# Performance work log

Hardware: AMD Instinct MI355X
Metric: run time of the kernel (lower is better)

## Reference

```python
import jax, jax.numpy as jnp
import numpy as np

N_NODES = 100000
N_EDGES = 1600000
N_GRAPHS = 256
DIMS = [128, 128, 128, 128]  # gcn_layers_dim -> 3 GCNConv layers


def setup_inputs() -> dict:
    key = jax.random.key(0)
    ks = jax.random.split(key, 12)
    inp = {
        "x": jax.random.normal(ks[0], (N_NODES, DIMS[0]), jnp.float32),
        "edge_index": jax.random.randint(ks[1], (2, N_EDGES), 0, N_NODES),
        "edge_weight": jax.random.uniform(ks[2], (N_EDGES,), jnp.float32),
        "batch": jnp.sort(jax.random.randint(ks[3], (N_NODES,), 0, N_GRAPHS)),
    }
    for i in range(3):
        fan_in = DIMS[i]
        scale = 1.0 / np.sqrt(fan_in)
        inp[f"W{i+1}"] = jax.random.uniform(ks[4 + 2 * i], (DIMS[i], DIMS[i + 1]),
                                             jnp.float32, -scale, scale)
        inp[f"b{i+1}"] = jax.random.uniform(ks[5 + 2 * i], (DIMS[i + 1],),
                                             jnp.float32, -scale, scale)
    return inp


def reference(x, edge_index, edge_weight, batch, W1, b1, W2, b2, W3, b3):
    n = x.shape[0]
    # PyG GCNConv: add self-loops with weight 1, symmetric normalization.
    loop = jnp.arange(n)
    row = jnp.concatenate([edge_index[0], loop])  # source nodes
    col = jnp.concatenate([edge_index[1], loop])  # target nodes (aggregation index)
    w = jnp.concatenate([edge_weight, jnp.ones((n,), x.dtype)])
    deg = jax.ops.segment_sum(w, col, num_segments=n)
    dinv = jnp.where(deg > 0, jax.lax.rsqrt(deg), jnp.zeros_like(deg))
    norm = dinv[row] * w * dinv[col]  # [E+N]

    # global_mean_pool setup
    counts = jax.ops.segment_sum(jnp.ones((n,), x.dtype), batch,
                                 num_segments=N_GRAPHS)
    counts = jnp.maximum(counts, 1.0)[:, None]

    def gcn_conv(h, W, b):
        hl = h @ W                      # linear projection first (PyG order)
        msg = hl[row] * norm[:, None]   # gather + edge scaling
        out = jax.ops.segment_sum(msg, col, num_segments=n)  # scatter-add
        return out + b

    embeddings = []
    h = x
    for W, b in ((W1, b1), (W2, b2), (W3, b3)):
        h = gcn_conv(h, W, b)
        h = jax.nn.relu(h)              # relu_layers_index = [0,1,2]
        emb = jax.ops.segment_sum(h, batch, num_segments=N_GRAPHS) / counts
        embeddings.append(emb)          # gep = global_mean_pool
    return tuple(embeddings)
```

## Files before the change

kernel.cpp:

```cpp
#include <hip/hip_runtime.h>


typedef short short8 __attribute__((ext_vector_type(8)));
typedef float f32x4  __attribute__((ext_vector_type(4)));

__device__ inline unsigned pack_bf16x2(float a, float b) {
    unsigned ua = __float_as_uint(a);
    ua = (ua + 0x7FFFu + ((ua >> 16) & 1u)) >> 16;
    unsigned ub = __float_as_uint(b);
    ub = (ub + 0x7FFFu + ((ub >> 16) & 1u)) >> 16;
    return ua | (ub << 16);
}
__device__ inline ushort bf16_1(float a) {
    unsigned ua = __float_as_uint(a);
    return (ushort)((ua + 0x7FFFu + ((ua >> 16) & 1u)) >> 16);
}
__device__ inline float bf_lo(unsigned u) { return __uint_as_float(u << 16); }
__device__ inline float bf_hi(unsigned u) { return __uint_as_float(u & 0xFFFF0000u); }

__global__ void k_prep(int* __restrict__ cnt, int N,
                       const int* __restrict__ batch, int* __restrict__ gb, int G,
                       const float* __restrict__ W0, const float* __restrict__ W1,
                       const float* __restrict__ W2, ushort* __restrict__ WbT) {
    int id = blockIdx.x * blockDim.x + threadIdx.x;
    if (id < N) cnt[id] = 0;
    if (id <= G) {
        int lo = 0, hi = N;
        while (lo < hi) { int mid = (lo + hi) >> 1; if (batch[mid] < id) lo = mid + 1; else hi = mid; }
        gb[id] = lo;
    }
    if (id < 3 * 16384) {
        int l = id >> 14;
        const float* W = (l == 0) ? W0 : ((l == 1) ? W1 : W2);
        int id2 = id & 16383;
        int n = id2 & 127, k = id2 >> 7;
        WbT[l * 16384 + n * 128 + k] = bf16_1(W[k * 128 + n]);
    }
}

__global__ void k_phase1(const int* __restrict__ ei, int* __restrict__ cnt,
                         int* __restrict__ epos, int E,
                         const float4* __restrict__ x4, uint2* __restrict__ xb2,
                         int nCast) {
    int tid = blockIdx.x * blockDim.x + threadIdx.x;
    if (tid < E) {
        int c = ei[E + tid];
        epos[tid] = atomicAdd(&cnt[c], 1);
    }
    int stride = gridDim.x * blockDim.x;
    for (int i = tid; i < nCast; i += stride) {
        float4 f = x4[i];
        uint2 v;
        v.x = pack_bf16x2(f.x, f.y);
        v.y = pack_bf16x2(f.z, f.w);
        xb2[i] = v;
    }
}

__global__ __launch_bounds__(1024) void k_scan1(const int* __restrict__ cnt,
                                                int* __restrict__ pre,
                                                int* __restrict__ bsum, int n) {
    __shared__ int wsum[16];
    int t = threadIdx.x, lane = t & 63, w = t >> 6;
    int i = blockIdx.x * 1024 + t;
    int v = (i < n) ? cnt[i] : 0;
    int x = v;
#pragma unroll
    for (int off = 1; off < 64; off <<= 1) {
        int y = __shfl_up(x, off, 64);
        if (lane >= off) x += y;
    }
    if (lane == 63) wsum[w] = x;
    __syncthreads();
    int woff = 0, tot = 0;
#pragma unroll
    for (int q = 0; q < 16; q++) { int s = wsum[q]; if (q < w) woff += s; tot += s; }
    if (i < n) pre[i] = woff + x - v;
    if (t == 0) bsum[blockIdx.x] = tot;
}

__global__ __launch_bounds__(128) void k_scan2(int* __restrict__ bsum, int nb,
                                               int* __restrict__ ptrv, int n) {
    __shared__ int ws[2];
    int t = threadIdx.x, lane = t & 63, w = t >> 6;
    int v = (t < nb) ? bsum[t] : 0;
    int x = v;
#pragma unroll
    for (int off = 1; off < 64; off <<= 1) {
        int y = __shfl_up(x, off, 64);
        if (lane >= off) x += y;
    }
    if (lane == 63) ws[w] = x;
    __syncthreads();
    int woff = (w == 1) ? ws[0] : 0;
    int tot = ws[0] + ws[1];
    if (t < nb) bsum[t] = woff + x - v;
    if (t == 0) ptrv[n] = tot;
}

__global__ void k_scatter(const int* __restrict__ ei, const float* __restrict__ ew,
                          const int* __restrict__ pre, const int* __restrict__ bsum,
                          int* __restrict__ ptrv, const int* __restrict__ epos,
                          int2* __restrict__ csr, int E, int N) {
    int e = blockIdx.x * blockDim.x + threadIdx.x;
    if (e < N) ptrv[e] = pre[e] + bsum[e >> 10];
    if (e >= E) return;
    int r = ei[e];
    int c = ei[E + e];
    int2 v; v.x = r; v.y = __float_as_int(ew[e]);
    csr[pre[c] + bsum[c >> 10] + epos[e]] = v;
}

__global__ __launch_bounds__(256) void k_degdinv(const int2* __restrict__ csr,
                                                 const int* __restrict__ ptrv,
                                                 float* __restrict__ dinv, int N) {
    int node = blockIdx.x * 8 + (threadIdx.x >> 5);
    int j = threadIdx.x & 31;
    if (node >= N) return;
    int e0 = ptrv[node], e1 = ptrv[node + 1];
    float s = (j == 0) ? 1.0f : 0.0f;
    for (int e = e0 + j; e < e1; e += 32) s += __int_as_float(csr[e].y);
#pragma unroll
    for (int off = 1; off < 32; off <<= 1) s += __shfl_xor(s, off, 64);
    if (j == 0) dinv[node] = rsqrtf(s);
}

__global__ __launch_bounds__(256) void k_norm(int2* __restrict__ csr,
                                              const int* __restrict__ ptrv,
                                              const float* __restrict__ dinv, int N) {
    int node = blockIdx.x * 8 + (threadIdx.x >> 5);
    int j = threadIdx.x & 31;
    if (node >= N) return;
    float dc = dinv[node];
    int e0 = ptrv[node], e1 = ptrv[node + 1];
    for (int e = e0 + j; e < e1; e += 32) {
        int2 m = csr[e];
        m.y = __float_as_int(dinv[m.x] * __int_as_float(m.y) * dc);
        csr[e] = m;
    }
}

__global__ __launch_bounds__(256) void k_gemm_mfma(const unsigned* __restrict__ Hb,
                                                   const ushort* __restrict__ WbT,
                                                   unsigned* __restrict__ O, int M) {
    __shared__ unsigned sOut[4 * 32 * 64];
    int lane = threadIdx.x & 63;
    int wv = threadIdx.x >> 6;
    int quad = lane >> 4;
    int mrow = lane & 15;
    int m0 = blockIdx.x * 128 + wv * 32;
    int r0 = m0 + mrow;
    int r1 = r0 + 16;
    int r0c = r0 < M ? r0 : M - 1;
    int r1c = r1 < M ? r1 : M - 1;

    short8 a0[4], a1[4];
#pragma unroll
    for (int s = 0; s < 4; s++) {
        a0[s] = *(const short8*)(Hb + (size_t)r0c * 64 + s * 16 + quad * 4);
        a1[s] = *(const short8*)(Hb + (size_t)r1c * 64 + s * 16 + quad * 4);
    }
    f32x4 acc0[8], acc1[8];
#pragma unroll
    for (int t = 0; t < 8; t++) {
        acc0[t] = (f32x4){0.f, 0.f, 0.f, 0.f};
        acc1[t] = (f32x4){0.f, 0.f, 0.f, 0.f};
    }
#pragma unroll
    for (int s = 0; s < 4; s++) {
#pragma unroll
        for (int t = 0; t < 8; t++) {
            short8 b = *(const short8*)(WbT + (t * 16 + mrow) * 128 + s * 32 + quad * 8);
            acc0[t] = __builtin_amdgcn_mfma_f32_16x16x32_bf16(a0[s], b, acc0[t], 0, 0, 0);
            acc1[t] = __builtin_amdgcn_mfma_f32_16x16x32_bf16(a1[s], b, acc1[t], 0, 0, 0);
        }
    }
    ushort* so = (ushort*)(sOut + wv * 32 * 64);
#pragma unroll
    for (int t = 0; t < 8; t++) {
#pragma unroll
        for (int r = 0; r < 4; r++) {
            int lr = quad * 4 + r;
            int c = t * 16 + mrow;
            so[lr * 128 + c] = bf16_1(acc0[t][r]);
            so[(lr + 16) * 128 + c] = bf16_1(acc1[t][r]);
        }
    }
    __syncthreads();
    const unsigned* si = sOut + wv * 32 * 64;
#pragma unroll 8
    for (int r = 0; r < 32; r++) {
        int row = m0 + r;
        if (row < M) O[(size_t)row * 64 + lane] = si[r * 64 + lane];
    }
}

__global__ __launch_bounds__(256) void k_agg(const unsigned* __restrict__ HL,
                                             const int* __restrict__ ptr,
                                             const int2* __restrict__ csr,
                                             const float* __restrict__ dinv,
                                             const float* __restrict__ bias,
                                             unsigned* __restrict__ Hout, int M) {
    __shared__ int2 sM[4 * 64];
    int node = (int)((blockIdx.x * blockDim.x + threadIdx.x) >> 6);
    if (node >= M) return;
    int lane = threadIdx.x & 63;
    int half = lane >> 5;
    int q = lane & 31;
    int2* mbase = &sM[(threadIdx.x >> 6) * 64];
    int e0 = ptr[node], e1 = ptr[node + 1];
    int deg = e1 - e0;
    int nbv = deg < 64 ? deg : 64;
    if (lane < nbv) mbase[lane] = csr[e0 + lane];
    const uint2* HL2 = (const uint2*)HL;
    float di = dinv[node];
    float sn = (half == 0) ? di * di : 0.f;
    uint2 us = HL2[(size_t)node * 32 + q];
    float a0 = sn * bf_lo(us.x), a1 = sn * bf_hi(us.x);
    float a2 = sn * bf_lo(us.y), a3 = sn * bf_hi(us.y);
    int j = half;
    for (; j + 16 <= nbv; j += 16) {
        int2 m[8]; uint2 u[8];
#pragma unroll
        for (int t = 0; t < 8; t++) m[t] = mbase[j + 2 * t];
#pragma unroll
        for (int t = 0; t < 8; t++) u[t] = HL2[(size_t)m[t].x * 32 + q];
#pragma unroll
        for (int t = 0; t < 8; t++) {
            float nv = __int_as_float(m[t].y);
            a0 += nv * bf_lo(u[t].x); a1 += nv * bf_hi(u[t].x);
            a2 += nv * bf_lo(u[t].y); a3 += nv * bf_hi(u[t].y);
        }
    }
    for (; j + 8 <= nbv; j += 8) {
        int2 m[4]; uint2 u[4];
#pragma unroll
        for (int t = 0; t < 4; t++) m[t] = mbase[j + 2 * t];
#pragma unroll
        for (int t = 0; t < 4; t++) u[t] = HL2[(size_t)m[t].x * 32 + q];
#pragma unroll
        for (int t = 0; t < 4; t++) {
            float nv = __int_as_float(m[t].y);
            a0 += nv * bf_lo(u[t].x); a1 += nv * bf_hi(u[t].x);
            a2 += nv * bf_lo(u[t].y); a3 += nv * bf_hi(u[t].y);
        }
    }
    for (; j < nbv; j += 2) {
        int2 m = mbase[j];
        uint2 u = HL2[(size_t)m.x * 32 + q];
        float nv = __int_as_float(m.y);
        a0 += nv * bf_lo(u.x); a1 += nv * bf_hi(u.x);
        a2 += nv * bf_lo(u.y); a3 += nv * bf_hi(u.y);
    }
    for (int e = e0 + 64 + half; e < e1; e += 2) {
        int2 m = csr[e];
        uint2 u = HL2[(size_t)m.x * 32 + q];
        float nv = __int_as_float(m.y);
        a0 += nv * bf_lo(u.x); a1 += nv * bf_hi(u.x);
        a2 += nv * bf_lo(u.y); a3 += nv * bf_hi(u.y);
    }
    a0 += __shfl_xor(a0, 32, 64);
    a1 += __shfl_xor(a1, 32, 64);
    a2 += __shfl_xor(a2, 32, 64);
    a3 += __shfl_xor(a3, 32, 64);
    float4 bv = ((const float4*)bias)[q];
    float r0 = fmaxf(a0 + bv.x, 0.f);
    float r1 = fmaxf(a1 + bv.y, 0.f);
    float r2 = fmaxf(a2 + bv.z, 0.f);
    float r3 = fmaxf(a3 + bv.w, 0.f);
    if (half == 0) {
        uint2 pv;
        pv.x = pack_bf16x2(r0, r1);
        pv.y = pack_bf16x2(r2, r3);
        ((uint2*)(Hout + (size_t)node * 64))[q] = pv;
    }
}

__global__ __launch_bounds__(256) void k_pool(const unsigned* __restrict__ HB,
                                              const int* __restrict__ gb,
                                              float* __restrict__ outp) {
    __shared__ float part[4][128];
    int g = blockIdx.x;
    int lane = threadIdx.x & 63, w = threadIdx.x >> 6;
    int s = gb[g], e = gb[g + 1];
    float ax = 0.f, ay = 0.f;
    for (int i = s + w; i < e; i += 4) {
        unsigned u = HB[(size_t)i * 64 + lane];
        ax += bf_lo(u); ay += bf_hi(u);
    }
    part[w][lane * 2] = ax;
    part[w][lane * 2 + 1] = ay;
    __syncthreads();
    if (threadIdx.x < 128) {
        float sum = part[0][threadIdx.x] + part[1][threadIdx.x]
                  + part[2][threadIdx.x] + part[3][threadIdx.x];
        float c = (float)(e - s);
        outp[g * 128 + threadIdx.x] = sum / fmaxf(c, 1.0f);
    }
}

extern "C" void kernel_launch(void* const* d_in, const int* in_sizes, int n_in,
                              void* d_out, int out_size, void* d_ws, size_t ws_size,
                              hipStream_t stream) {
    const float* x     = (const float*)d_in[0];
    const int*   ei    = (const int*)d_in[1];
    const float* ew    = (const float*)d_in[2];
    const int*   batch = (const int*)d_in[3];
    const float* Wt[3] = {(const float*)d_in[4], (const float*)d_in[6], (const float*)d_in[8]};
    const float* bt[3] = {(const float*)d_in[5], (const float*)d_in[7], (const float*)d_in[9]};
    float* out = (float*)d_out;

    const int D = 128;
    const int N = in_sizes[0] / D;
    const int E = in_sizes[2];
    const int G = out_size / (3 * D);

    char* p = (char*)d_ws;
    auto alloc = [&](size_t bytes) {
        void* r = (void*)p;
        p += (bytes + 255) & ~(size_t)255;
        return r;
    };
    int*      cnt    = (int*)alloc((size_t)N * 4);
    int*      ptr    = (int*)alloc((size_t)(N + 1) * 4);
    int*      pre    = (int*)alloc((size_t)N * 4);
    int*      bsum   = (int*)alloc((size_t)128 * 4);
    int*      gb     = (int*)alloc((size_t)(G + 1) * 4);
    float*    dinv   = (float*)alloc((size_t)N * 4);
    ushort*   WbT    = (ushort*)alloc((size_t)3 * 16384 * 2);
    int2*     csr    = (int2*)alloc((size_t)E * 8);
    unsigned* xb     = (unsigned*)alloc((size_t)N * 64 * 4);
    unsigned* bufHL  = (unsigned*)alloc((size_t)N * 64 * 4);
    unsigned* bufH   = (unsigned*)alloc((size_t)N * 64 * 4);
    int*      epos   = (int*)bufH;

    int nb = (N + 1023) / 1024;
    int prepWork = N > 3 * 16384 ? N : 3 * 16384;

    k_prep<<<(prepWork + 255) / 256, 256, 0, stream>>>(cnt, N, batch, gb, G,
                                                       Wt[0], Wt[1], Wt[2], WbT);
    k_phase1<<<(E + 255) / 256, 256, 0, stream>>>(ei, cnt, epos, E,
                                                  (const float4*)x, (uint2*)xb, N * 32);
    k_scan1<<<nb, 1024, 0, stream>>>(cnt, pre, bsum, N);
    k_scan2<<<1, 128, 0, stream>>>(bsum, nb, ptr, N);
    k_scatter<<<(E + 255) / 256, 256, 0, stream>>>(ei, ew, pre, bsum, ptr, epos,
                                                   csr, E, N);
    k_degdinv<<<(N + 7) / 8, 256, 0, stream>>>(csr, ptr, dinv, N);
    k_norm<<<(N + 7) / 8, 256, 0, stream>>>(csr, ptr, dinv, N);

    for (int l = 0; l < 3; l++) {
        const unsigned* hin = (l == 0) ? xb : bufH;
        k_gemm_mfma<<<(N + 127) / 128, 256, 0, stream>>>(hin, WbT + (size_t)l * 16384,
                                                         bufHL, N);
        k_agg<<<(N + 3) / 4, 256, 0, stream>>>(bufHL, ptr, csr, dinv, bt[l], bufH, N);
        k_pool<<<G, 256, 0, stream>>>(bufH, gb, out + (size_t)l * G * D);
    }
}
```

Before: 613.2 us.

## Fuse first GEMM with edge counting, merge scan2 into scatter, co-launch GEMM and pool

The separate fp32-to-bf16 cast pass over x is removed. The layer-0 GEMM now reads fp32 x directly, converts it in registers, and runs in the same grid as the edge-count atomics. The second scan stage is folded into the scatter kernel, with each block redundantly re-scanning the 128 block sums. Each later layer's GEMM shares one launch with the previous layer's pooling. The 16-wide unrolled edge loop in aggregation is also dropped. Together these cut launches and a full-size intermediate buffer round-trip, at the cost of heterogeneous blocks in the fused grids and a smaller unroll in the gather loop.

```diff
diff --git a/kernel.cpp b/kernel.cpp
--- a/kernel.cpp
+++ b/kernel.cpp
@@ -18,12 +18,111 @@
 __device__ inline float bf_lo(unsigned u) { return __uint_as_float(u << 16); }
 __device__ inline float bf_hi(unsigned u) { return __uint_as_float(u & 0xFFFF0000u); }
 
-__global__ void k_prep(int* __restrict__ cnt, int N,
+
+template <bool F32IN>
+__device__ __forceinline__ void gemm_tile(const void* __restrict__ Hin,
+                                          const ushort* __restrict__ WbT,
+                                          unsigned* __restrict__ O, int M,
+                                          int bid, unsigned* sOut) {
+    int lane = threadIdx.x & 63;
+    int wv = threadIdx.x >> 6;
+    int quad = lane >> 4;
+    int mrow = lane & 15;
+    int m0 = bid * 128 + wv * 32;
+    int r0 = m0 + mrow;
+    int r1 = r0 + 16;
+    int r0c = r0 < M ? r0 : M - 1;
+    int r1c = r1 < M ? r1 : M - 1;
+
+    short8 a0[4], a1[4];
+    if (F32IN) {
+        const float* Hf = (const float*)Hin;
+#pragma unroll
+        for (int s = 0; s < 4; s++) {
+            const float4* p0 = (const float4*)(Hf + (size_t)r0c * 128 + s * 32 + quad * 8);
+            const float4* p1 = (const float4*)(Hf + (size_t)r1c * 128 + s * 32 + quad * 8);
+            float4 f0 = p0[0], f1 = p0[1];
+            float4 g0 = p1[0], g1 = p1[1];
+            union { short8 s8; unsigned u[4]; } t0, t1;
+            t0.u[0] = pack_bf16x2(f0.x, f0.y); t0.u[1] = pack_bf16x2(f0.z, f0.w);
+            t0.u[2] = pack_bf16x2(f1.x, f1.y); t0.u[3] = pack_bf16x2(f1.z, f1.w);
+            t1.u[0] = pack_bf16x2(g0.x, g0.y); t1.u[1] = pack_bf16x2(g0.z, g0.w);
+            t1.u[2] = pack_bf16x2(g1.x, g1.y); t1.u[3] = pack_bf16x2(g1.z, g1.w);
+            a0[s] = t0.s8; a1[s] = t1.s8;
+        }
+    } else {
+        const unsigned* Hb = (const unsigned*)Hin;
+#pragma unroll
+        for (int s = 0; s < 4; s++) {
+            a0[s] = *(const short8*)(Hb + (size_t)r0c * 64 + s * 16 + quad * 4);
+            a1[s] = *(const short8*)(Hb + (size_t)r1c * 64 + s * 16 + quad * 4);
+        }
+    }
+    f32x4 acc0[8], acc1[8];
+#pragma unroll
+    for (int t = 0; t < 8; t++) {
+        acc0[t] = (f32x4){0.f, 0.f, 0.f, 0.f};
+        acc1[t] = (f32x4){0.f, 0.f, 0.f, 0.f};
+    }
+#pragma unroll
+    for (int s = 0; s < 4; s++) {
+#pragma unroll
+        for (int t = 0; t < 8; t++) {
+            short8 b = *(const short8*)(WbT + (t * 16 + mrow) * 128 + s * 32 + quad * 8);
+            acc0[t] = __builtin_amdgcn_mfma_f32_16x16x32_bf16(a0[s], b, acc0[t], 0, 0, 0);
+            acc1[t] = __builtin_amdgcn_mfma_f32_16x16x32_bf16(a1[s], b, acc1[t], 0, 0, 0);
+        }
+    }
+    ushort* so = (ushort*)(sOut + wv * 32 * 64);
+#pragma unroll
+    for (int t = 0; t < 8; t++) {
+#pragma unroll
+        for (int r = 0; r < 4; r++) {
+            int lr = quad * 4 + r;
+            int c = t * 16 + mrow;
+            so[lr * 128 + c] = bf16_1(acc0[t][r]);
+            so[(lr + 16) * 128 + c] = bf16_1(acc1[t][r]);
+        }
+    }
+    __syncthreads();
+    const unsigned* si = sOut + wv * 32 * 64;
+#pragma unroll 8
+    for (int r = 0; r < 32; r++) {
+        int row = m0 + r;
+        if (row < M) O[(size_t)row * 64 + lane] = si[r * 64 + lane];
+    }
+}
+
+__device__ __forceinline__ void pool_tile(const unsigned* __restrict__ HB,
+                                          const int* __restrict__ gb,
+                                          float* __restrict__ outp, int g,
+                                          float* part) {
+    int lane = threadIdx.x & 63, w = threadIdx.x >> 6;
+    int s = gb[g], e = gb[g + 1];
+    float ax = 0.f, ay = 0.f;
+    for (int i = s + w; i < e; i += 4) {
+        unsigned u = HB[(size_t)i * 64 + lane];
+        ax += bf_lo(u); ay += bf_hi(u);
+    }
+    part[w * 128 + lane * 2] = ax;
+    part[w * 128 + lane * 2 + 1] = ay;
+    __syncthreads();
+    if (threadIdx.x < 128) {
+        float sum = part[threadIdx.x] + part[128 + threadIdx.x]
+                  + part[256 + threadIdx.x] + part[384 + threadIdx.x];
+        float c = (float)(e - s);
+        outp[g * 128 + threadIdx.x] = sum / fmaxf(c, 1.0f);
+    }
+}
+
+
+__global__ void k_prep(int* __restrict__ cnt, int N, int* __restrict__ bsum,
                        const int* __restrict__ batch, int* __restrict__ gb, int G,
                        const float* __restrict__ W0, const float* __restrict__ W1,
                        const float* __restrict__ W2, ushort* __restrict__ WbT) {
     int id = blockIdx.x * blockDim.x + threadIdx.x;
     if (id < N) cnt[id] = 0;
+    if (id < 128) bsum[id] = 0;
     if (id <= G) {
         int lo = 0, hi = N;
         while (lo < hi) { int mid = (lo + hi) >> 1; if (batch[mid] < id) lo = mid + 1; else hi = mid; }
@@ -38,22 +137,22 @@
     }
 }
 
-__global__ void k_phase1(const int* __restrict__ ei, int* __restrict__ cnt,
-                         int* __restrict__ epos, int E,
-                         const float4* __restrict__ x4, uint2* __restrict__ xb2,
-                         int nCast) {
-    int tid = blockIdx.x * blockDim.x + threadIdx.x;
+__global__ __launch_bounds__(256) void k_phase1(const int* __restrict__ ei,
+                                                int* __restrict__ cnt,
+                                                int* __restrict__ epos, int E,
+                                                const float* __restrict__ x,
+                                                const ushort* __restrict__ WbT,
+                                                unsigned* __restrict__ O, int M,
+                                                int nbGemm) {
+    __shared__ unsigned sBuf[8192];
+    if (blockIdx.x < nbGemm) {
+        gemm_tile<true>(x, WbT, O, M, blockIdx.x, sBuf);
+        return;
+    }
+    int tid = (blockIdx.x - nbGemm) * 256 + threadIdx.x;
     if (tid < E) {
         int c = ei[E + tid];
         epos[tid] = atomicAdd(&cnt[c], 1);
-    }
-    int stride = gridDim.x * blockDim.x;
-    for (int i = tid; i < nCast; i += stride) {
-        float4 f = x4[i];
-        uint2 v;
-        v.x = pack_bf16x2(f.x, f.y);
-        v.y = pack_bf16x2(f.z, f.w);
-        xb2[i] = v;
     }
 }
 
@@ -79,36 +178,42 @@
     if (t == 0) bsum[blockIdx.x] = tot;
 }
 
-__global__ __launch_bounds__(128) void k_scan2(int* __restrict__ bsum, int nb,
-                                               int* __restrict__ ptrv, int n) {
-    __shared__ int ws[2];
-    int t = threadIdx.x, lane = t & 63, w = t >> 6;
-    int v = (t < nb) ? bsum[t] : 0;
+__global__ __launch_bounds__(256) void k_scatter(const int* __restrict__ ei,
+                                                 const float* __restrict__ ew,
+                                                 const int* __restrict__ pre,
+                                                 const int* __restrict__ bsumRaw,
+                                                 int* __restrict__ ptrv,
+                                                 const int* __restrict__ epos,
+                                                 int2* __restrict__ csr, int E, int N) {
+    __shared__ int sRaw[256];
+    __shared__ int sPre[256];
+    __shared__ int sWt[4];
+    int t = threadIdx.x;
+    sRaw[t] = (t < 128) ? bsumRaw[t] : 0;
+    __syncthreads();
+    int lane = t & 63, w2 = t >> 6;
+    int v = sRaw[t];
     int x = v;
 #pragma unroll
     for (int off = 1; off < 64; off <<= 1) {
         int y = __shfl_up(x, off, 64);
         if (lane >= off) x += y;
     }
-    if (lane == 63) ws[w] = x;
-    __syncthreads();
-    int woff = (w == 1) ? ws[0] : 0;
-    int tot = ws[0] + ws[1];
-    if (t < nb) bsum[t] = woff + x - v;
-    if (t == 0) ptrv[n] = tot;
-}
-
-__global__ void k_scatter(const int* __restrict__ ei, const float* __restrict__ ew,
-                          const int* __restrict__ pre, const int* __restrict__ bsum,
-                          int* __restrict__ ptrv, const int* __restrict__ epos,
-                          int2* __restrict__ csr, int E, int N) {
-    int e = blockIdx.x * blockDim.x + threadIdx.x;
-    if (e < N) ptrv[e] = pre[e] + bsum[e >> 10];
+    if (lane == 63) sWt[w2] = x;
+    __syncthreads();
+    int base = 0;
+#pragma unroll
+    for (int q = 0; q < 4; q++) { if (q < w2) base += sWt[q]; }
+    sPre[t] = base + x - v;
+    __syncthreads();
+    int e = blockIdx.x * 256 + t;
+    if (e < N) ptrv[e] = pre[e] + sPre[e >> 10];
+    if (e == 0) ptrv[N] = sWt[0] + sWt[1];
     if (e >= E) return;
     int r = ei[e];
     int c = ei[E + e];
-    int2 v; v.x = r; v.y = __float_as_int(ew[e]);
-    csr[pre[c] + bsum[c >> 10] + epos[e]] = v;
+    int2 mv; mv.x = r; mv.y = __float_as_int(ew[e]);
+    csr[pre[c] + sPre[c >> 10] + epos[e]] = mv;
 }
 
 __global__ __launch_bounds__(256) void k_degdinv(const int2* __restrict__ csr,
@@ -137,61 +242,6 @@
         int2 m = csr[e];
         m.y = __float_as_int(dinv[m.x] * __int_as_float(m.y) * dc);
         csr[e] = m;
-    }
-}
-
-__global__ __launch_bounds__(256) void k_gemm_mfma(const unsigned* __restrict__ Hb,
-                                                   const ushort* __restrict__ WbT,
-                                                   unsigned* __restrict__ O, int M) {
-    __shared__ unsigned sOut[4 * 32 * 64];
-    int lane = threadIdx.x & 63;
-    int wv = threadIdx.x >> 6;
-    int quad = lane >> 4;
-    int mrow = lane & 15;
-    int m0 = blockIdx.x * 128 + wv * 32;
-    int r0 = m0 + mrow;
-    int r1 = r0 + 16;
-    int r0c = r0 < M ? r0 : M - 1;
-    int r1c = r1 < M ? r1 : M - 1;
-
-    short8 a0[4], a1[4];
-#pragma unroll
-    for (int s = 0; s < 4; s++) {
-        a0[s] = *(const short8*)(Hb + (size_t)r0c * 64 + s * 16 + quad * 4);
-        a1[s] = *(const short8*)(Hb + (size_t)r1c * 64 + s * 16 + quad * 4);
-    }
-    f32x4 acc0[8], acc1[8];
-#pragma unroll
-    for (int t = 0; t < 8; t++) {
-        acc0[t] = (f32x4){0.f, 0.f, 0.f, 0.f};
-        acc1[t] = (f32x4){0.f, 0.f, 0.f, 0.f};
-    }
-#pragma unroll
-    for (int s = 0; s < 4; s++) {
-#pragma unroll
-        for (int t = 0; t < 8; t++) {
-            short8 b = *(const short8*)(WbT + (t * 16 + mrow) * 128 + s * 32 + quad * 8);
-            acc0[t] = __builtin_amdgcn_mfma_f32_16x16x32_bf16(a0[s], b, acc0[t], 0, 0, 0);
-            acc1[t] = __builtin_amdgcn_mfma_f32_16x16x32_bf16(a1[s], b, acc1[t], 0, 0, 0);
-        }
-    }
-    ushort* so = (ushort*)(sOut + wv * 32 * 64);
-#pragma unroll
-    for (int t = 0; t < 8; t++) {
-#pragma unroll
-        for (int r = 0; r < 4; r++) {
-            int lr = quad * 4 + r;
-            int c = t * 16 + mrow;
-            so[lr * 128 + c] = bf16_1(acc0[t][r]);
-            so[(lr + 16) * 128 + c] = bf16_1(acc1[t][r]);
-        }
-    }
-    __syncthreads();
-    const unsigned* si = sOut + wv * 32 * 64;
-#pragma unroll 8
-    for (int r = 0; r < 32; r++) {
-        int row = m0 + r;
-        if (row < M) O[(size_t)row * 64 + lane] = si[r * 64 + lane];
     }
 }
 
@@ -219,19 +269,6 @@
     float a0 = sn * bf_lo(us.x), a1 = sn * bf_hi(us.x);
     float a2 = sn * bf_lo(us.y), a3 = sn * bf_hi(us.y);
     int j = half;
-    for (; j + 16 <= nbv; j += 16) {
-        int2 m[8]; uint2 u[8];
-#pragma unroll
-        for (int t = 0; t < 8; t++) m[t] = mbase[j + 2 * t];
-#pragma unroll
-        for (int t = 0; t < 8; t++) u[t] = HL2[(size_t)m[t].x * 32 + q];
-#pragma unroll
-        for (int t = 0; t < 8; t++) {
-            float nv = __int_as_float(m[t].y);
-            a0 += nv * bf_lo(u[t].x); a1 += nv * bf_hi(u[t].x);
-            a2 += nv * bf_lo(u[t].y); a3 += nv * bf_hi(u[t].y);
-        }
-    }
     for (; j + 8 <= nbv; j += 8) {
         int2 m[4]; uint2 u[4];
 #pragma unroll
@@ -276,27 +313,18 @@
     }
 }
 
-__global__ __launch_bounds__(256) void k_pool(const unsigned* __restrict__ HB,
-                                              const int* __restrict__ gb,
-                                              float* __restrict__ outp) {
-    __shared__ float part[4][128];
-    int g = blockIdx.x;
-    int lane = threadIdx.x & 63, w = threadIdx.x >> 6;
-    int s = gb[g], e = gb[g + 1];
-    float ax = 0.f, ay = 0.f;
-    for (int i = s + w; i < e; i += 4) {
-        unsigned u = HB[(size_t)i * 64 + lane];
-        ax += bf_lo(u); ay += bf_hi(u);
-    }
-    part[w][lane * 2] = ax;
-    part[w][lane * 2 + 1] = ay;
-    __syncthreads();
-    if (threadIdx.x < 128) {
-        float sum = part[0][threadIdx.x] + part[1][threadIdx.x]
-                  + part[2][threadIdx.x] + part[3][threadIdx.x];
-        float c = (float)(e - s);
-        outp[g * 128 + threadIdx.x] = sum / fmaxf(c, 1.0f);
-    }
+__global__ __launch_bounds__(256) void k_gemm_pool(const unsigned* __restrict__ Hb,
+                                                   const ushort* __restrict__ WbT,
+                                                   unsigned* __restrict__ O, int M,
+                                                   const int* __restrict__ gb,
+                                                   float* __restrict__ outp,
+                                                   int nbGemm) {
+    __shared__ unsigned sBuf[8192];
+    if (blockIdx.x < nbGemm) {
+        gemm_tile<false>(Hb, WbT, O, M, blockIdx.x, sBuf);
+        return;
+    }
+    pool_tile(Hb, gb, outp, blockIdx.x - nbGemm, (float*)sBuf);
 }
 
 extern "C" void kernel_launch(void* const* d_in, const int* in_sizes, int n_in,
@@ -329,30 +357,32 @@
     float*    dinv   = (float*)alloc((size_t)N * 4);
     ushort*   WbT    = (ushort*)alloc((size_t)3 * 16384 * 2);
     int2*     csr    = (int2*)alloc((size_t)E * 8);
-    unsigned* xb     = (unsigned*)alloc((size_t)N * 64 * 4);
     unsigned* bufHL  = (unsigned*)alloc((size_t)N * 64 * 4);
     unsigned* bufH   = (unsigned*)alloc((size_t)N * 64 * 4);
     int*      epos   = (int*)bufH;
 
     int nb = (N + 1023) / 1024;
+    int nbGemm = (N + 127) / 128;
+    int nbAtomic = (E + 255) / 256;
     int prepWork = N > 3 * 16384 ? N : 3 * 16384;
 
-    k_prep<<<(prepWork + 255) / 256, 256, 0, stream>>>(cnt, N, batch, gb, G,
+    k_prep<<<(prepWork + 255) / 256, 256, 0, stream>>>(cnt, N, bsum, batch, gb, G,
                                                        Wt[0], Wt[1], Wt[2], WbT);
-    k_phase1<<<(E + 255) / 256, 256, 0, stream>>>(ei, cnt, epos, E,
-                                                  (const float4*)x, (uint2*)xb, N * 32);
+    k_phase1<<<nbGemm + nbAtomic, 256, 0, stream>>>(ei, cnt, epos, E,
+                                                    x, WbT, bufHL, N, nbGemm);
     k_scan1<<<nb, 1024, 0, stream>>>(cnt, pre, bsum, N);
-    k_scan2<<<1, 128, 0, stream>>>(bsum, nb, ptr, N);
     k_scatter<<<(E + 255) / 256, 256, 0, stream>>>(ei, ew, pre, bsum, ptr, epos,
                                                    csr, E, N);
     k_degdinv<<<(N + 7) / 8, 256, 0, stream>>>(csr, ptr, dinv, N);
     k_norm<<<(N + 7) / 8, 256, 0, stream>>>(csr, ptr, dinv, N);
 
-    for (int l = 0; l < 3; l++) {
-        const unsigned* hin = (l == 0) ? xb : bufH;
-        k_gemm_mfma<<<(N + 127) / 128, 256, 0, stream>>>(hin, WbT + (size_t)l * 16384,
-                                                         bufHL, N);
-        k_agg<<<(N + 3) / 4, 256, 0, stream>>>(bufHL, ptr, csr, dinv, bt[l], bufH, N);
-        k_pool<<<G, 256, 0, stream>>>(bufH, gb, out + (size_t)l * G * D);
-    }
-}
+    k_agg<<<(N + 3) / 4, 256, 0, stream>>>(bufHL, ptr, csr, dinv, bt[0], bufH, N);
+    k_gemm_pool<<<nbGemm + G, 256, 0, stream>>>(bufH, WbT + 16384, bufHL, N,
+                                                gb, out + 0 * (size_t)G * D, nbGemm);
+    k_agg<<<(N + 3) / 4, 256, 0, stream>>>(bufHL, ptr, csr, dinv, bt[1], bufH, N);
+    k_gemm_pool<<<nbGemm + G, 256, 0, stream>>>(bufH, WbT + 2 * 16384, bufHL, N,
+                                                gb, out + 1 * (size_t)G * D, nbGemm);
+    k_agg<<<(N + 3) / 4, 256, 0, stream>>>(bufHL, ptr, csr, dinv, bt[2], bufH, N);
+    k_gemm_pool<<<G, 256, 0, stream>>>(bufH, WbT, nullptr, 0,
+                                       gb, out + 2 * (size_t)G * D, 0);
+}
```

Result: faster. 568.2 us (-7.3%).
